# Kernel tuning notes

Hardware: AMD Instinct MI355X
Metric: run time of the kernel (lower is better)

## Reference

```python
import jax, jax.numpy as jnp
import numpy as np

B, S, D, H = 2, 2048, 1024, 16
E = D // H  # depth per head = 64


def setup_inputs() -> dict:
    key = jax.random.key(0)
    ks = jax.random.split(key, 11)
    scale = 0.02
    return {
        "q": jax.random.normal(ks[0], (B, S, D), jnp.float32),
        "k": jax.random.normal(ks[1], (B, S, D), jnp.float32),
        "v": jax.random.normal(ks[2], (B, S, D), jnp.float32),
        # per-head projection weights, stacked over heads: [H, D, E]
        "Wq": jax.random.normal(ks[3], (H, D, E), jnp.float32) * scale,
        "bq": jax.random.normal(ks[4], (H, E), jnp.float32) * scale,
        "Wk": jax.random.normal(ks[5], (H, D, E), jnp.float32) * scale,
        "bk": jax.random.normal(ks[6], (H, E), jnp.float32) * scale,
        "Wv": jax.random.normal(ks[7], (H, D, E), jnp.float32) * scale,
        "bv": jax.random.normal(ks[8], (H, E), jnp.float32) * scale,
        "Wo": jax.random.normal(ks[9], (D, D), jnp.float32) * scale,
        "bo": jax.random.normal(ks[10], (D,), jnp.float32) * scale,
    }


def reference(q, k, v, Wq, bq, Wk, bk, Wv, bv, Wo, bo):
    # Batched QKV projections (replaces the per-head Python loop): [B,H,S,E]
    qh = jnp.einsum("bsd,hde->bhse", q, Wq) + bq[None, :, None, :]
    kh = jnp.einsum("bsd,hde->bhse", k, Wk) + bk[None, :, None, :]
    vh = jnp.einsum("bsd,hde->bhse", v, Wv) + bv[None, :, None, :]

    # scaled dot-product attention with causal (triu, diagonal=1) mask
    scores = jnp.einsum("bhqe,bhke->bhqk", qh, kh) / jnp.sqrt(
        jnp.asarray(E, jnp.float32)
    )
    Sq, Sk = scores.shape[-2], scores.shape[-1]
    causal = jnp.triu(jnp.ones((Sq, Sk), bool), k=1)  # True above diagonal
    scores = jnp.where(causal[None, None], -jnp.inf, scores)
    weights = jax.nn.softmax(scores, axis=-1)  # [B,H,S,S]

    attn = jnp.einsum("bhqk,bhke->bhqe", weights, vh)  # [B,H,S,E]
    concat = attn.transpose(0, 2, 1, 3).reshape(attn.shape[0], attn.shape[2], -1)
    out = concat @ Wo + bo  # final linear [B,S,D]
    return out, weights
```

## Files before the change

kernel.cpp:

```cpp
#include <hip/hip_runtime.h>
#include <math.h>

#define B_ 2
#define S_ 2048
#define D_ 1024
#define H_ 16
#define E_ 64
#define Z_ (B_ * H_)
#define QBLK 128
#define NEG_BIG (-1e30f)

typedef short short8 __attribute__((ext_vector_type(8)));
typedef float f32x4 __attribute__((ext_vector_type(4)));

__device__ __forceinline__ ushort f2bf(float x) {
    union { float f; unsigned u; } c; c.f = x;
    unsigned r = (c.u + 0x7FFFu + ((c.u >> 16) & 1u)) >> 16;
    return (ushort)r;
}

__device__ __forceinline__ f32x4 mfma16(short8 a, short8 b, f32x4 c) {
    return __builtin_amdgcn_mfma_f32_16x16x32_bf16(a, b, c, 0, 0, 0);
}

__global__ __launch_bounds__(256) void cvt3_kernel(
    const float* __restrict__ in0, const float* __restrict__ in1,
    const float* __restrict__ in2, ushort* __restrict__ out0,
    ushort* __restrict__ out1, ushort* __restrict__ out2, int n4) {
    const int which = blockIdx.y;
    const float* in = (which == 0) ? in0 : (which == 1) ? in1 : in2;
    ushort* out = (which == 0) ? out0 : (which == 1) ? out1 : out2;
    int i = blockIdx.x * 256 + threadIdx.x;
    if (i < n4) {
        float4 x = reinterpret_cast<const float4*>(in)[i];
        ushort4 p;
        p.x = f2bf(x.x); p.y = f2bf(x.y); p.z = f2bf(x.z); p.w = f2bf(x.w);
        reinterpret_cast<ushort4*>(out)[i] = p;
    }
}

__global__ __launch_bounds__(256) void wtrans3_kernel(
    const float* __restrict__ w0, const float* __restrict__ w1,
    const float* __restrict__ w2, ushort* __restrict__ o0,
    ushort* __restrict__ o1, ushort* __restrict__ o2) {
    __shared__ float tile[32][33];
    const int zz = blockIdx.z;
    const int which = zz >> 4, h = zz & 15;
    const float* in = (which == 0) ? w0 : (which == 1) ? w1 : w2;
    ushort* out = (which == 0) ? o0 : (which == 1) ? o1 : o2;
    const int K = D_, N = E_;
    const float* ins = in + (size_t)h * K * N;
    ushort* outs = out + (size_t)h * K * N;
    const int k0 = blockIdx.x * 32, n0 = blockIdx.y * 32;
    const int tx = threadIdx.x & 31, ty = threadIdx.x >> 5;
#pragma unroll
    for (int r = 0; r < 32; r += 8)
        tile[ty + r][tx] = ins[(size_t)(k0 + ty + r) * N + n0 + tx];
    __syncthreads();
#pragma unroll
    for (int r = 0; r < 32; r += 8)
        outs[(size_t)(n0 + ty + r) * K + k0 + tx] = f2bf(tile[tx][ty + r]);
}

__global__ __launch_bounds__(256) void wtrans_kernel(
    const float* __restrict__ in, ushort* __restrict__ out, int K, int N) {
    __shared__ float tile[32][33];
    const int k0 = blockIdx.x * 32, n0 = blockIdx.y * 32;
    const int tx = threadIdx.x & 31, ty = threadIdx.x >> 5;
#pragma unroll
    for (int r = 0; r < 32; r += 8)
        tile[ty + r][tx] = in[(size_t)(k0 + ty + r) * N + n0 + tx];
    __syncthreads();
#pragma unroll
    for (int r = 0; r < 32; r += 8)
        out[(size_t)(n0 + ty + r) * K + k0 + tx] = f2bf(tile[tx][ty + r]);
}

__global__ __launch_bounds__(512) void proj3_mfma_kernel(
    const ushort* __restrict__ xq, const ushort* __restrict__ xk,
    const ushort* __restrict__ xv, const ushort* __restrict__ Wqt,
    const ushort* __restrict__ Wkt, const ushort* __restrict__ Wvt,
    const float* __restrict__ bq, const float* __restrict__ bk,
    const float* __restrict__ bv, ushort* __restrict__ qh,
    ushort* __restrict__ kh, ushort* __restrict__ vt, float qscale) {
    const int bid = blockIdx.x;
    const int which = bid >> 8;
    const int inner = bid & 255;
    const ushort* Xb = (which == 0) ? xq : (which == 1) ? xk : xv;
    const ushort* Wt = (which == 0) ? Wqt : (which == 1) ? Wkt : Wvt;
    const float* bias = (which == 0) ? bq : (which == 1) ? bk : bv;
    ushort* out = (which == 0) ? qh : (which == 1) ? kh : vt;
    const float oscale = (which == 0) ? qscale : 1.0f;

    const int w = (inner & 7) * 32 + (inner >> 3);
    const int mt = w >> 3, nt = w & 7;
    const int gm0 = mt * 128, n0 = nt * 128;
    const int t = threadIdx.x;
    const int wv = t >> 6, l = t & 63, j = l & 15, g = l >> 4;
    const int wm = wv >> 2, wn = wv & 3;

    __shared__ int4 Xs[2][1024];
    __shared__ int4 Ws[2][1024];

    const f32x4 zf = {0.f, 0.f, 0.f, 0.f};
    f32x4 acc[4][2];
#pragma unroll
    for (int mm = 0; mm < 4; ++mm) { acc[mm][0] = zf; acc[mm][1] = zf; }

    const int rr0 = t >> 3, bb0 = t & 7;
    const int rr1 = (t + 512) >> 3, bb1 = t & 7;
    const int slot0 = rr0 * 8 + (bb0 ^ (rr0 & 7));
    const int slot1 = rr1 * 8 + (bb1 ^ (rr1 & 7));

    Xs[0][slot0] = *reinterpret_cast<const int4*>(Xb + (size_t)(gm0 + rr0) * D_ + bb0 * 8);
    Ws[0][slot0] = *reinterpret_cast<const int4*>(Wt + (size_t)(n0 + rr0) * D_ + bb0 * 8);
    Xs[0][slot1] = *reinterpret_cast<const int4*>(Xb + (size_t)(gm0 + rr1) * D_ + bb1 * 8);
    Ws[0][slot1] = *reinterpret_cast<const int4*>(Wt + (size_t)(n0 + rr1) * D_ + bb1 * 8);
    __syncthreads();

    for (int ks = 0; ks < 16; ++ks) {
        const int cur = ks & 1;
        const bool pf = (ks < 15);
        int4 xr0, wr0, xr1, wr1;
        if (pf) {
            const int k0n = (ks + 1) * 64;
            xr0 = *reinterpret_cast<const int4*>(Xb + (size_t)(gm0 + rr0) * D_ + k0n + bb0 * 8);
            wr0 = *reinterpret_cast<const int4*>(Wt + (size_t)(n0 + rr0) * D_ + k0n + bb0 * 8);
            xr1 = *reinterpret_cast<const int4*>(Xb + (size_t)(gm0 + rr1) * D_ + k0n + bb1 * 8);
            wr1 = *reinterpret_cast<const int4*>(Wt + (size_t)(n0 + rr1) * D_ + k0n + bb1 * 8);
        }

        __builtin_amdgcn_s_setprio(1);
#pragma unroll
        for (int eh = 0; eh < 2; ++eh) {
            short8 bfr[2];
#pragma unroll
            for (int nn = 0; nn < 2; ++nn) {
                int e = wn * 32 + nn * 16 + j;
                bfr[nn] = *reinterpret_cast<const short8*>(
                    &Ws[cur][e * 8 + ((eh * 4 + g) ^ (e & 7))]);
            }
#pragma unroll
            for (int mm = 0; mm < 4; ++mm) {
                int arow = wm * 64 + mm * 16 + j;
                short8 a = *reinterpret_cast<const short8*>(
                    &Xs[cur][arow * 8 + ((eh * 4 + g) ^ (arow & 7))]);
                acc[mm][0] = mfma16(a, bfr[0], acc[mm][0]);
                acc[mm][1] = mfma16(a, bfr[1], acc[mm][1]);
            }
        }
        __builtin_amdgcn_s_setprio(0);

        if (pf) {
            Xs[cur ^ 1][slot0] = xr0; Ws[cur ^ 1][slot0] = wr0;
            Xs[cur ^ 1][slot1] = xr1; Ws[cur ^ 1][slot1] = wr1;
        }
        __syncthreads();
    }

#pragma unroll
    for (int nn = 0; nn < 2; ++nn) {
        const int ncol = n0 + wn * 32 + nn * 16 + j;
        const int h = ncol >> 6, col = ncol & 63;
        const float bvv = bias[ncol];
#pragma unroll
        for (int mm = 0; mm < 4; ++mm) {
            const int m = gm0 + wm * 64 + mm * 16 + g * 4;
            const int b = m >> 11, s = m & 2047;
            if (which != 2) {
#pragma unroll
                for (int r = 0; r < 4; ++r)
                    out[((size_t)(b * H_ + h) * S_ + s + r) * E_ + col] =
                        f2bf((acc[mm][nn][r] + bvv) * oscale);
            } else {
                ushort4 pk;
                pk.x = f2bf(acc[mm][nn][0] + bvv);
                pk.y = f2bf(acc[mm][nn][1] + bvv);
                pk.z = f2bf(acc[mm][nn][2] + bvv);
                pk.w = f2bf(acc[mm][nn][3] + bvv);
                *reinterpret_cast<ushort4*>(
                    &out[((size_t)(b * H_ + h) * E_ + col) * S_ + s]) = pk;
            }
        }
    }
}

__global__ __launch_bounds__(512) void attn_fused_kernel(
    const ushort* __restrict__ qh, const ushort* __restrict__ kh,
    const ushort* __restrict__ vt, float* __restrict__ wts,
    ushort* __restrict__ attnc) {
    const int f = blockIdx.x;
    const int xcd = f & 7, w = f >> 3;
    const int z = xcd * 4 + (w >> 4);
    const int qt = w & 15;
    const int q0 = qt * QBLK;
    const int ktmax = 2 * qt + 1;

    const int t = threadIdx.x;
    const int wv = t >> 6, l = t & 63, j = l & 15, g = l >> 4;

    const ushort* qhz = qh + (size_t)z * S_ * E_;
    const ushort* khz = kh + (size_t)z * S_ * E_;
    const ushort* vtz = vt + (size_t)z * E_ * S_;
    float* wz = wts + (size_t)z * S_ * S_;

    __shared__ int4 Kb[2][512];
    __shared__ int4 Vb[2][512];
    __shared__ __align__(16) ushort Ps[8][16][72];

    const int rr = t >> 3, bb = t & 7;
    const int lds_i = rr * 8 + (bb ^ (rr & 7));
    const int koff = rr * 64 + bb * 8;
    const int voff = rr * 2048 + bb * 8;

    short8 qf[2];
    {
        const ushort* qrow = qhz + (size_t)(q0 + wv * 16 + j) * E_;
        qf[0] = *reinterpret_cast<const short8*>(qrow + g * 8);
        qf[1] = *reinterpret_cast<const short8*>(qrow + 32 + g * 8);
    }
    const int qr_base = q0 + wv * 16 + g * 4;

    const f32x4 zf = {0.f, 0.f, 0.f, 0.f};
    float lsum[4] = {0.f, 0.f, 0.f, 0.f};

    Kb[0][lds_i] = *reinterpret_cast<const int4*>(khz + koff);
    __syncthreads();
    for (int kt = 0; kt <= ktmax; ++kt) {
        const int cur = kt & 1;
        const bool pf = (kt < ktmax);
        int4 kreg;
        if (pf)
            kreg = *reinterpret_cast<const int4*>(khz + (kt + 1) * 4096 + koff);

        f32x4 sacc[4];
#pragma unroll
        for (int n = 0; n < 4; ++n) sacc[n] = zf;
        __builtin_amdgcn_s_setprio(1);
#pragma unroll
        for (int eh = 0; eh < 2; ++eh) {
#pragma unroll
            for (int n = 0; n < 4; ++n) {
                const int kc = n * 16 + j;
                short8 kf = *reinterpret_cast<const short8*>(
                    &Kb[cur][kc * 8 + ((eh * 4 + g) ^ (j & 7))]);
                sacc[n] = mfma16(qf[eh], kf, sacc[n]);
            }
        }
        __builtin_amdgcn_s_setprio(0);

        if (kt >= 2 * qt) {
#pragma unroll
            for (int n = 0; n < 4; ++n) {
                const int col = kt * 64 + n * 16 + j;
#pragma unroll
                for (int r = 0; r < 4; ++r)
                    if (col > qr_base + r) sacc[n][r] = NEG_BIG;
            }
        }
#pragma unroll
        for (int r = 0; r < 4; ++r)
            lsum[r] += (exp2f(sacc[0][r]) + exp2f(sacc[1][r])) +
                       (exp2f(sacc[2][r]) + exp2f(sacc[3][r]));

        if (pf) Kb[cur ^ 1][lds_i] = kreg;
        __syncthreads();
    }

    float invl[4];
#pragma unroll
    for (int r = 0; r < 4; ++r) {
        float tt = lsum[r];
        tt += __shfl_xor(tt, 1);
        tt += __shfl_xor(tt, 2);
        tt += __shfl_xor(tt, 4);
        tt += __shfl_xor(tt, 8);
        invl[r] = 1.0f / tt;
    }

    f32x4 oacc[4];
#pragma unroll
    for (int n = 0; n < 4; ++n) oacc[n] = zf;

    Kb[0][lds_i] = *reinterpret_cast<const int4*>(khz + koff);
    Vb[0][lds_i] = *reinterpret_cast<const int4*>(vtz + voff);
    __syncthreads();
    for (int kt = 0; kt <= ktmax; ++kt) {
        const int cur = kt & 1;
        const bool pf = (kt < ktmax);
        int4 kreg, vreg;
        if (pf) {
            kreg = *reinterpret_cast<const int4*>(khz + (kt + 1) * 4096 + koff);
            vreg = *reinterpret_cast<const int4*>(vtz + (kt + 1) * 64 + voff);
        }

        f32x4 sacc[4];
#pragma unroll
        for (int n = 0; n < 4; ++n) sacc[n] = zf;
        __builtin_amdgcn_s_setprio(1);
#pragma unroll
        for (int eh = 0; eh < 2; ++eh) {
#pragma unroll
            for (int n = 0; n < 4; ++n) {
                const int kc = n * 16 + j;
                short8 kf = *reinterpret_cast<const short8*>(
                    &Kb[cur][kc * 8 + ((eh * 4 + g) ^ (j & 7))]);
                sacc[n] = mfma16(qf[eh], kf, sacc[n]);
            }
        }
        __builtin_amdgcn_s_setprio(0);

        if (kt >= 2 * qt) {
#pragma unroll
            for (int n = 0; n < 4; ++n) {
                const int col = kt * 64 + n * 16 + j;
#pragma unroll
                for (int r = 0; r < 4; ++r)
                    if (col > qr_base + r) sacc[n][r] = NEG_BIG;
            }
        }

#pragma unroll
        for (int n = 0; n < 4; ++n) {
#pragma unroll
            for (int r = 0; r < 4; ++r) {
                float p = exp2f(sacc[n][r]) * invl[r];
                wz[(size_t)(qr_base + r) * S_ + kt * 64 + n * 16 + j] = p;
                Ps[wv][g * 4 + r][n * 16 + j] = f2bf(p);
            }
        }

        __builtin_amdgcn_s_setprio(1);
#pragma unroll
        for (int ks = 0; ks < 2; ++ks) {
            short8 pa =
                *reinterpret_cast<const short8*>(&Ps[wv][j][ks * 32 + g * 8]);
#pragma unroll
            for (int n = 0; n < 4; ++n) {
                const int e = n * 16 + j;
                short8 vb = *reinterpret_cast<const short8*>(
                    &Vb[cur][e * 8 + ((ks * 4 + g) ^ (j & 7))]);
                oacc[n] = mfma16(pa, vb, oacc[n]);
            }
        }
        __builtin_amdgcn_s_setprio(0);

        if (pf) {
            Kb[cur ^ 1][lds_i] = kreg;
            Vb[cur ^ 1][lds_i] = vreg;
        }
        __syncthreads();
    }

    {
        const int b = z >> 4, hh = z & 15;
#pragma unroll
        for (int n = 0; n < 4; ++n)
#pragma unroll
            for (int r = 0; r < 4; ++r)
                attnc[((size_t)(b * S_ + qr_base + r)) * D_ + hh * E_ +
                      n * 16 + j] = f2bf(oacc[n][r]);
    }

    const int c0 = q0 + QBLK;
    const int w4 = (S_ - c0) >> 2;
    if (w4 > 0) {
        const float4 z4 = make_float4(0.f, 0.f, 0.f, 0.f);
        for (int row = 0; row < QBLK; ++row) {
            float4* rp =
                reinterpret_cast<float4*>(wz + (size_t)(q0 + row) * S_ + c0);
            for (int c = t; c < w4; c += 512) rp[c] = z4;
        }
    }
}

__global__ __launch_bounds__(512) void outproj_mfma_kernel(
    const ushort* __restrict__ A, const ushort* __restrict__ Wot,
    const float* __restrict__ bo, float* __restrict__ out) {
    const int bid = blockIdx.x;
    const int w = (bid & 7) * 32 + (bid >> 3);
    const int mt = w >> 3, nt = w & 7;
    const int gm0 = mt * 128, n0 = nt * 128;
    const int t = threadIdx.x;
    const int wv = t >> 6, l = t & 63, j = l & 15, g = l >> 4;
    const int wm = wv >> 2, wn = wv & 3;

    __shared__ int4 As[2][1024];
    __shared__ int4 Bs[2][1024];

    const f32x4 zf = {0.f, 0.f, 0.f, 0.f};
    f32x4 acc[4][2];
#pragma unroll
    for (int mm = 0; mm < 4; ++mm) { acc[mm][0] = zf; acc[mm][1] = zf; }

    const int rr0 = t >> 3, bb0 = t & 7;
    const int rr1 = (t + 512) >> 3, bb1 = t & 7;
    const int slot0 = rr0 * 8 + (bb0 ^ (rr0 & 7));
    const int slot1 = rr1 * 8 + (bb1 ^ (rr1 & 7));

    As[0][slot0] = *reinterpret_cast<const int4*>(A + (size_t)(gm0 + rr0) * D_ + bb0 * 8);
    Bs[0][slot0] = *reinterpret_cast<const int4*>(Wot + (size_t)(n0 + rr0) * D_ + bb0 * 8);
    As[0][slot1] = *reinterpret_cast<const int4*>(A + (size_t)(gm0 + rr1) * D_ + bb1 * 8);
    Bs[0][slot1] = *reinterpret_cast<const int4*>(Wot + (size_t)(n0 + rr1) * D_ + bb1 * 8);
    __syncthreads();

    for (int ks = 0; ks < 16; ++ks) {
        const int cur = ks & 1;
        const bool pf = (ks < 15);
        int4 ar0, br0, ar1, br1;
        if (pf) {
            const int k0n = (ks + 1) * 64;
            ar0 = *reinterpret_cast<const int4*>(A + (size_t)(gm0 + rr0) * D_ + k0n + bb0 * 8);
            br0 = *reinterpret_cast<const int4*>(Wot + (size_t)(n0 + rr0) * D_ + k0n + bb0 * 8);
            ar1 = *reinterpret_cast<const int4*>(A + (size_t)(gm0 + rr1) * D_ + k0n + bb1 * 8);
            br1 = *reinterpret_cast<const int4*>(Wot + (size_t)(n0 + rr1) * D_ + k0n + bb1 * 8);
        }

        __builtin_amdgcn_s_setprio(1);
#pragma unroll
        for (int eh = 0; eh < 2; ++eh) {
            short8 bfr[2];
#pragma unroll
            for (int nn = 0; nn < 2; ++nn) {
                int e = wn * 32 + nn * 16 + j;
                bfr[nn] = *reinterpret_cast<const short8*>(
                    &Bs[cur][e * 8 + ((eh * 4 + g) ^ (e & 7))]);
            }
#pragma unroll
            for (int mm = 0; mm < 4; ++mm) {
                int arow = wm * 64 + mm * 16 + j;
                short8 a = *reinterpret_cast<const short8*>(
                    &As[cur][arow * 8 + ((eh * 4 + g) ^ (arow & 7))]);
                acc[mm][0] = mfma16(a, bfr[0], acc[mm][0]);
                acc[mm][1] = mfma16(a, bfr[1], acc[mm][1]);
            }
        }
        __builtin_amdgcn_s_setprio(0);

        if (pf) {
            As[cur ^ 1][slot0] = ar0; Bs[cur ^ 1][slot0] = br0;
            As[cur ^ 1][slot1] = ar1; Bs[cur ^ 1][slot1] = br1;
        }
        __syncthreads();
    }

#pragma unroll
    for (int nn = 0; nn < 2; ++nn) {
        const int ncol = n0 + wn * 32 + nn * 16 + j;
        const float bvv = bo[ncol];
#pragma unroll
        for (int mm = 0; mm < 4; ++mm) {
            const int m = gm0 + wm * 64 + mm * 16 + g * 4;
#pragma unroll
            for (int r = 0; r < 4; ++r)
                out[(size_t)(m + r) * D_ + ncol] = acc[mm][nn][r] + bvv;
        }
    }
}

extern "C" void kernel_launch(void* const* d_in, const int* in_sizes, int n_in,
                              void* d_out, int out_size, void* d_ws,
                              size_t ws_size, hipStream_t stream) {
    const float* q = (const float*)d_in[0];
    const float* k = (const float*)d_in[1];
    const float* v = (const float*)d_in[2];
    const float* Wq = (const float*)d_in[3];
    const float* bq = (const float*)d_in[4];
    const float* Wk = (const float*)d_in[5];
    const float* bk = (const float*)d_in[6];
    const float* Wv = (const float*)d_in[7];
    const float* bv = (const float*)d_in[8];
    const float* Wo = (const float*)d_in[9];
    const float* bo = (const float*)d_in[10];

    float* out = (float*)d_out;
    float* wts = out + (size_t)B_ * S_ * D_;

    const size_t NZ = (size_t)Z_ * S_ * E_;
    const size_t NW = (size_t)H_ * E_ * D_;
    ushort* qh = (ushort*)d_ws;
    ushort* kh = qh + NZ;
    ushort* vt = kh + NZ;
    ushort* attnc = vt + NZ;
    ushort* Wqt = attnc + NZ;
    ushort* Wkt = Wqt + NW;
    ushort* Wvt = Wkt + NW;
    ushort* Wot = Wvt + NW;

    ushort* xq = (ushort*)wts;
    ushort* xk = xq + NZ;
    ushort* xv = xk + NZ;

    const float QSCALE = 0.125f * 1.44269504088896340736f;
    const int n4 = (int)(NZ / 4);

    dim3 b256(256), b512(512);
    cvt3_kernel<<<dim3(4096, 3), b256, 0, stream>>>(q, k, v, xq, xk, xv, n4);
    wtrans3_kernel<<<dim3(32, 2, 48), b256, 0, stream>>>(Wq, Wk, Wv, Wqt, Wkt,
                                                         Wvt);
    wtrans_kernel<<<dim3(32, 32, 1), b256, 0, stream>>>(Wo, Wot, D_, D_);
    proj3_mfma_kernel<<<dim3(768), b512, 0, stream>>>(
        xq, xk, xv, Wqt, Wkt, Wvt, bq, bk, bv, qh, kh, vt, QSCALE);
    attn_fused_kernel<<<dim3(512), b512, 0, stream>>>(qh, kh, vt, wts, attnc);
    outproj_mfma_kernel<<<dim3(256), b512, 0, stream>>>(attnc, Wot, bo, out);
}
```

Before: 243.0 us.

## Stage GEMM and attention tiles via direct global-to-LDS loads, nontemporal weight stores

Replaces register-staged prefetch (global load into VGPRs, then LDS store) with global_load_lds direct-to-LDS copies in the projection, attention and output-projection kernels. The swizzle moves to the global source addresses, so each wave writes a contiguous LDS chunk. The large attention-weights output and its zero fill now use nontemporal stores, bf16 conversion switches to a cheaper round-half-up, and launch bounds request two blocks per CU. The aim is to cut VGPR pressure, free issue slots and avoid cache pollution from the weights write. The fast rounding differs slightly from round-to-nearest-even, and correctness depends on the asynchronous LDS fill being complete by the existing barriers.

```diff
diff --git a/kernel.cpp b/kernel.cpp
--- a/kernel.cpp
+++ b/kernel.cpp
@@ -18,9 +18,19 @@
     unsigned r = (c.u + 0x7FFFu + ((c.u >> 16) & 1u)) >> 16;
     return (ushort)r;
 }
+__device__ __forceinline__ ushort f2bf_fast(float x) {
+    union { float f; unsigned u; } c; c.f = x;
+    return (ushort)((c.u + 0x8000u) >> 16);
+}
 
 __device__ __forceinline__ f32x4 mfma16(short8 a, short8 b, f32x4 c) {
     return __builtin_amdgcn_mfma_f32_16x16x32_bf16(a, b, c, 0, 0, 0);
+}
+
+__device__ __forceinline__ void gload16(const void* g, void* l) {
+    __builtin_amdgcn_global_load_lds(
+        (const __attribute__((address_space(1))) void*)g,
+        (__attribute__((address_space(3))) void*)l, 16, 0, 0);
 }
 
 __global__ __launch_bounds__(256) void cvt3_kernel(
@@ -76,7 +86,7 @@
         out[(size_t)(n0 + ty + r) * K + k0 + tx] = f2bf(tile[tx][ty + r]);
 }
 
-__global__ __launch_bounds__(512) void proj3_mfma_kernel(
+__global__ __launch_bounds__(512, 2) void proj3_mfma_kernel(
     const ushort* __restrict__ xq, const ushort* __restrict__ xk,
     const ushort* __restrict__ xv, const ushort* __restrict__ Wqt,
     const ushort* __restrict__ Wkt, const ushort* __restrict__ Wvt,
@@ -107,28 +117,28 @@
 #pragma unroll
     for (int mm = 0; mm < 4; ++mm) { acc[mm][0] = zf; acc[mm][1] = zf; }
 
-    const int rr0 = t >> 3, bb0 = t & 7;
-    const int rr1 = (t + 512) >> 3, bb1 = t & 7;
-    const int slot0 = rr0 * 8 + (bb0 ^ (rr0 & 7));
-    const int slot1 = rr1 * 8 + (bb1 ^ (rr1 & 7));
-
-    Xs[0][slot0] = *reinterpret_cast<const int4*>(Xb + (size_t)(gm0 + rr0) * D_ + bb0 * 8);
-    Ws[0][slot0] = *reinterpret_cast<const int4*>(Wt + (size_t)(n0 + rr0) * D_ + bb0 * 8);
-    Xs[0][slot1] = *reinterpret_cast<const int4*>(Xb + (size_t)(gm0 + rr1) * D_ + bb1 * 8);
-    Ws[0][slot1] = *reinterpret_cast<const int4*>(Wt + (size_t)(n0 + rr1) * D_ + bb1 * 8);
+    const int s0 = t, s1 = t + 512;
+    const int r0 = s0 >> 3, c0 = (s0 & 7) ^ (r0 & 7);
+    const int r1 = s1 >> 3, c1 = (s1 & 7) ^ (r1 & 7);
+    const size_t xo0 = (size_t)(gm0 + r0) * D_ + c0 * 8;
+    const size_t xo1 = (size_t)(gm0 + r1) * D_ + c1 * 8;
+    const size_t wo0 = (size_t)(n0 + r0) * D_ + c0 * 8;
+    const size_t wo1 = (size_t)(n0 + r1) * D_ + c1 * 8;
+
+#define P3_STAGE(buf, kk)                                \
+    do {                                                 \
+        gload16(Xb + xo0 + (kk), &Xs[buf][wv * 64]);     \
+        gload16(Xb + xo1 + (kk), &Xs[buf][512 + wv * 64]); \
+        gload16(Wt + wo0 + (kk), &Ws[buf][wv * 64]);     \
+        gload16(Wt + wo1 + (kk), &Ws[buf][512 + wv * 64]); \
+    } while (0)
+
+    P3_STAGE(0, 0);
     __syncthreads();
 
     for (int ks = 0; ks < 16; ++ks) {
         const int cur = ks & 1;
-        const bool pf = (ks < 15);
-        int4 xr0, wr0, xr1, wr1;
-        if (pf) {
-            const int k0n = (ks + 1) * 64;
-            xr0 = *reinterpret_cast<const int4*>(Xb + (size_t)(gm0 + rr0) * D_ + k0n + bb0 * 8);
-            wr0 = *reinterpret_cast<const int4*>(Wt + (size_t)(n0 + rr0) * D_ + k0n + bb0 * 8);
-            xr1 = *reinterpret_cast<const int4*>(Xb + (size_t)(gm0 + rr1) * D_ + k0n + bb1 * 8);
-            wr1 = *reinterpret_cast<const int4*>(Wt + (size_t)(n0 + rr1) * D_ + k0n + bb1 * 8);
-        }
+        if (ks < 15) P3_STAGE(cur ^ 1, (ks + 1) * 64);
 
         __builtin_amdgcn_s_setprio(1);
 #pragma unroll
@@ -150,13 +160,9 @@
             }
         }
         __builtin_amdgcn_s_setprio(0);
-
-        if (pf) {
-            Xs[cur ^ 1][slot0] = xr0; Ws[cur ^ 1][slot0] = wr0;
-            Xs[cur ^ 1][slot1] = xr1; Ws[cur ^ 1][slot1] = wr1;
-        }
         __syncthreads();
     }
+#undef P3_STAGE
 
 #pragma unroll
     for (int nn = 0; nn < 2; ++nn) {
@@ -185,7 +191,7 @@
     }
 }
 
-__global__ __launch_bounds__(512) void attn_fused_kernel(
+__global__ __launch_bounds__(512, 2) void attn_fused_kernel(
     const ushort* __restrict__ qh, const ushort* __restrict__ kh,
     const ushort* __restrict__ vt, float* __restrict__ wts,
     ushort* __restrict__ attnc) {
@@ -208,10 +214,12 @@
     __shared__ int4 Vb[2][512];
     __shared__ __align__(16) ushort Ps[8][16][72];
 
-    const int rr = t >> 3, bb = t & 7;
-    const int lds_i = rr * 8 + (bb ^ (rr & 7));
-    const int koff = rr * 64 + bb * 8;
-    const int voff = rr * 2048 + bb * 8;
+    const int rr = t >> 3, bb = (t & 7) ^ ((t >> 3) & 7);
+    const size_t koff = (size_t)rr * 64 + bb * 8;
+    const size_t voff = (size_t)rr * 2048 + bb * 8;
+
+#define STAGE_K(buf, kt) gload16(khz + (size_t)(kt) * 4096 + koff, &Kb[buf][wv * 64])
+#define STAGE_V(buf, kt) gload16(vtz + (size_t)(kt) * 64 + voff, &Vb[buf][wv * 64])
 
     short8 qf[2];
     {
@@ -224,14 +232,11 @@
     const f32x4 zf = {0.f, 0.f, 0.f, 0.f};
     float lsum[4] = {0.f, 0.f, 0.f, 0.f};
 
-    Kb[0][lds_i] = *reinterpret_cast<const int4*>(khz + koff);
+    STAGE_K(0, 0);
     __syncthreads();
     for (int kt = 0; kt <= ktmax; ++kt) {
         const int cur = kt & 1;
-        const bool pf = (kt < ktmax);
-        int4 kreg;
-        if (pf)
-            kreg = *reinterpret_cast<const int4*>(khz + (kt + 1) * 4096 + koff);
+        if (kt < ktmax) STAGE_K(cur ^ 1, kt + 1);
 
         f32x4 sacc[4];
 #pragma unroll
@@ -263,7 +268,6 @@
             lsum[r] += (exp2f(sacc[0][r]) + exp2f(sacc[1][r])) +
                        (exp2f(sacc[2][r]) + exp2f(sacc[3][r]));
 
-        if (pf) Kb[cur ^ 1][lds_i] = kreg;
         __syncthreads();
     }
 
@@ -282,16 +286,14 @@
 #pragma unroll
     for (int n = 0; n < 4; ++n) oacc[n] = zf;
 
-    Kb[0][lds_i] = *reinterpret_cast<const int4*>(khz + koff);
-    Vb[0][lds_i] = *reinterpret_cast<const int4*>(vtz + voff);
+    STAGE_K(0, 0);
+    STAGE_V(0, 0);
     __syncthreads();
     for (int kt = 0; kt <= ktmax; ++kt) {
         const int cur = kt & 1;
-        const bool pf = (kt < ktmax);
-        int4 kreg, vreg;
-        if (pf) {
-            kreg = *reinterpret_cast<const int4*>(khz + (kt + 1) * 4096 + koff);
-            vreg = *reinterpret_cast<const int4*>(vtz + (kt + 1) * 64 + voff);
+        if (kt < ktmax) {
+            STAGE_K(cur ^ 1, kt + 1);
+            STAGE_V(cur ^ 1, kt + 1);
         }
 
         f32x4 sacc[4];
@@ -325,8 +327,9 @@
 #pragma unroll
             for (int r = 0; r < 4; ++r) {
                 float p = exp2f(sacc[n][r]) * invl[r];
-                wz[(size_t)(qr_base + r) * S_ + kt * 64 + n * 16 + j] = p;
-                Ps[wv][g * 4 + r][n * 16 + j] = f2bf(p);
+                __builtin_nontemporal_store(
+                    p, wz + (size_t)(qr_base + r) * S_ + kt * 64 + n * 16 + j);
+                Ps[wv][g * 4 + r][n * 16 + j] = f2bf_fast(p);
             }
         }
 
@@ -345,12 +348,10 @@
         }
         __builtin_amdgcn_s_setprio(0);
 
-        if (pf) {
-            Kb[cur ^ 1][lds_i] = kreg;
-            Vb[cur ^ 1][lds_i] = vreg;
-        }
         __syncthreads();
     }
+#undef STAGE_K
+#undef STAGE_V
 
     {
         const int b = z >> 4, hh = z & 15;
@@ -359,22 +360,23 @@
 #pragma unroll
             for (int r = 0; r < 4; ++r)
                 attnc[((size_t)(b * S_ + qr_base + r)) * D_ + hh * E_ +
-                      n * 16 + j] = f2bf(oacc[n][r]);
+                      n * 16 + j] = f2bf_fast(oacc[n][r]);
     }
 
     const int c0 = q0 + QBLK;
     const int w4 = (S_ - c0) >> 2;
     if (w4 > 0) {
-        const float4 z4 = make_float4(0.f, 0.f, 0.f, 0.f);
+        const f32x4 z4 = {0.f, 0.f, 0.f, 0.f};
         for (int row = 0; row < QBLK; ++row) {
-            float4* rp =
-                reinterpret_cast<float4*>(wz + (size_t)(q0 + row) * S_ + c0);
-            for (int c = t; c < w4; c += 512) rp[c] = z4;
-        }
-    }
-}
-
-__global__ __launch_bounds__(512) void outproj_mfma_kernel(
+            f32x4* rp =
+                reinterpret_cast<f32x4*>(wz + (size_t)(q0 + row) * S_ + c0);
+            for (int c = t; c < w4; c += 512)
+                __builtin_nontemporal_store(z4, rp + c);
+        }
+    }
+}
+
+__global__ __launch_bounds__(512, 2) void outproj_mfma_kernel(
     const ushort* __restrict__ A, const ushort* __restrict__ Wot,
     const float* __restrict__ bo, float* __restrict__ out) {
     const int bid = blockIdx.x;
@@ -393,28 +395,28 @@
 #pragma unroll
     for (int mm = 0; mm < 4; ++mm) { acc[mm][0] = zf; acc[mm][1] = zf; }
 
-    const int rr0 = t >> 3, bb0 = t & 7;
-    const int rr1 = (t + 512) >> 3, bb1 = t & 7;
-    const int slot0 = rr0 * 8 + (bb0 ^ (rr0 & 7));
-    const int slot1 = rr1 * 8 + (bb1 ^ (rr1 & 7));
-
-    As[0][slot0] = *reinterpret_cast<const int4*>(A + (size_t)(gm0 + rr0) * D_ + bb0 * 8);
-    Bs[0][slot0] = *reinterpret_cast<const int4*>(Wot + (size_t)(n0 + rr0) * D_ + bb0 * 8);
-    As[0][slot1] = *reinterpret_cast<const int4*>(A + (size_t)(gm0 + rr1) * D_ + bb1 * 8);
-    Bs[0][slot1] = *reinterpret_cast<const int4*>(Wot + (size_t)(n0 + rr1) * D_ + bb1 * 8);
+    const int s0 = t, s1 = t + 512;
+    const int r0 = s0 >> 3, c0 = (s0 & 7) ^ (r0 & 7);
+    const int r1 = s1 >> 3, c1 = (s1 & 7) ^ (r1 & 7);
+    const size_t ao0 = (size_t)(gm0 + r0) * D_ + c0 * 8;
+    const size_t ao1 = (size_t)(gm0 + r1) * D_ + c1 * 8;
+    const size_t bo0 = (size_t)(n0 + r0) * D_ + c0 * 8;
+    const size_t bo1 = (size_t)(n0 + r1) * D_ + c1 * 8;
+
+#define OP_STAGE(buf, kk)                                 \
+    do {                                                  \
+        gload16(A + ao0 + (kk), &As[buf][wv * 64]);       \
+        gload16(A + ao1 + (kk), &As[buf][512 + wv * 64]); \
+        gload16(Wot + bo0 + (kk), &Bs[buf][wv * 64]);     \
+        gload16(Wot + bo1 + (kk), &Bs[buf][512 + wv * 64]); \
+    } while (0)
+
+    OP_STAGE(0, 0);
     __syncthreads();
 
     for (int ks = 0; ks < 16; ++ks) {
         const int cur = ks & 1;
-        const bool pf = (ks < 15);
-        int4 ar0, br0, ar1, br1;
-        if (pf) {
-            const int k0n = (ks + 1) * 64;
-            ar0 = *reinterpret_cast<const int4*>(A + (size_t)(gm0 + rr0) * D_ + k0n + bb0 * 8);
-            br0 = *reinterpret_cast<const int4*>(Wot + (size_t)(n0 + rr0) * D_ + k0n + bb0 * 8);
-            ar1 = *reinterpret_cast<const int4*>(A + (size_t)(gm0 + rr1) * D_ + k0n + bb1 * 8);
-            br1 = *reinterpret_cast<const int4*>(Wot + (size_t)(n0 + rr1) * D_ + k0n + bb1 * 8);
-        }
+        if (ks < 15) OP_STAGE(cur ^ 1, (ks + 1) * 64);
 
         __builtin_amdgcn_s_setprio(1);
 #pragma unroll
@@ -436,13 +438,9 @@
             }
         }
         __builtin_amdgcn_s_setprio(0);
-
-        if (pf) {
-            As[cur ^ 1][slot0] = ar0; Bs[cur ^ 1][slot0] = br0;
-            As[cur ^ 1][slot1] = ar1; Bs[cur ^ 1][slot1] = br1;
-        }
         __syncthreads();
     }
+#undef OP_STAGE
 
 #pragma unroll
     for (int nn = 0; nn < 2; ++nn) {
```

Measured after the change: 261.3 us. 7.6% more time.
